# Kernel optimization log

Measured on AMD Instinct MI355X. Metric: run time of the kernel, lower is better.

The kernel has to match this reference:

```python
import jax, jax.numpy as jnp
import numpy as np
import math

D_MODEL = 256
D_STATE = 16
D_CONV = 4
EXPAND = 2
D_INNER = EXPAND * D_MODEL          # 512
DT_RANK = math.ceil(D_MODEL / 16)   # 16
EPS = 1e-5


def rmsnorm(x, w):
    return x * jax.lax.rsqrt(jnp.mean(x * x, axis=-1, keepdims=True) + EPS) * w


def mamba_mixer(x, in_proj, conv_w, conv_b, x_proj, dt_w, dt_b, A_log, Dp, out_proj):
    # x: [B, L, d_model]
    Bsz, L, _ = x.shape
    xz = x @ in_proj.T                       # [B, L, 2*d_inner]
    xh, z = jnp.split(xz, 2, axis=-1)        # each [B, L, d_inner]
    # causal depthwise conv1d over time (d_conv=4)
    xp = jnp.pad(xh, ((0, 0), (D_CONV - 1, 0), (0, 0)))
    xc = sum(xp[:, k:k + L, :] * conv_w[:, k] for k in range(D_CONV)) + conv_b
    xc = jax.nn.silu(xc)                     # [B, L, d_inner]
    x_dbl = xc @ x_proj.T                    # [B, L, dt_rank + 2*d_state]
    dt, Bm, Cm = jnp.split(x_dbl, [DT_RANK, DT_RANK + D_STATE], axis=-1)
    delta = jax.nn.softplus(dt @ dt_w.T + dt_b)   # [B, L, d_inner]
    A = -jnp.exp(A_log)                      # [d_inner, d_state]
    dA = jnp.exp(jnp.einsum('bld,dn->lbdn', delta, A))        # [L,B,d,n]
    dBu = jnp.einsum('bld,bln,bld->lbdn', delta, Bm, xc)       # [L,B,d,n]

    def step(h, inp):
        a, b = inp
        h = a * h + b
        return h, h

    h0 = jnp.zeros((Bsz, D_INNER, D_STATE), xc.dtype)
    _, hs = jax.lax.scan(step, h0, (dA, dBu))                  # [L,B,d,n]
    y = jnp.einsum('lbdn,bln->bld', hs, Cm) + xc * Dp          # [B,L,d_inner]
    y = y * jax.nn.silu(z)
    return y @ out_proj.T                                      # [B,L,d_model]


def block(x, norm_w, in_proj, conv_w, conv_b, x_proj, dt_w, dt_b, A_log, Dp, out_proj):
    # Block with fused_add_norm=False, residual=None: residual = x, h = mixer(norm(x))
    residual = x
    h = mamba_mixer(rmsnorm(x, norm_w), in_proj, conv_w, conv_b, x_proj,
                    dt_w, dt_b, A_log, Dp, out_proj)
    return h + residual


def setup_inputs() -> dict:
    key = jax.random.key(0)
    ks = jax.random.split(key, 16)
    B, L = 4, 2048

    def n(k, shape, s=0.02):
        return jax.random.normal(k, shape, jnp.float32) * s

    inp = {"x": jax.random.normal(ks[0], (B, L, D_MODEL), jnp.float32)}
    i = 1
    for pre in ("fw", "bw"):
        inp[pre + "_norm"] = jnp.ones((D_MODEL,), jnp.float32)
        inp[pre + "_in_proj"] = n(ks[i], (2 * D_INNER, D_MODEL)); i += 1
        inp[pre + "_conv_w"] = n(ks[i], (D_INNER, D_CONV), 0.1); i += 1
        inp[pre + "_conv_b"] = jnp.zeros((D_INNER,), jnp.float32)
        inp[pre + "_x_proj"] = n(ks[i], (DT_RANK + 2 * D_STATE, D_INNER)); i += 1
        inp[pre + "_dt_w"] = n(ks[i], (D_INNER, DT_RANK), 0.1); i += 1
        inp[pre + "_dt_b"] = n(ks[i], (D_INNER,), 0.1); i += 1
        inp[pre + "_A_log"] = jnp.log(jnp.tile(jnp.arange(1, D_STATE + 1, dtype=jnp.float32), (D_INNER, 1)))
        inp[pre + "_D"] = jnp.ones((D_INNER,), jnp.float32)
        inp[pre + "_out_proj"] = n(ks[i], (D_MODEL, D_INNER)); i += 1
    return inp


def reference(x,
              fw_norm, fw_in_proj, fw_conv_w, fw_conv_b, fw_x_proj, fw_dt_w, fw_dt_b, fw_A_log, fw_D, fw_out_proj,
              bw_norm, bw_in_proj, bw_conv_w, bw_conv_b, bw_x_proj, bw_dt_w, bw_dt_b, bw_A_log, bw_D, bw_out_proj):
    fwd = block(x, fw_norm, fw_in_proj, fw_conv_w, fw_conv_b, fw_x_proj,
                fw_dt_w, fw_dt_b, fw_A_log, fw_D, fw_out_proj)
    xb = jnp.flip(x, axis=1)
    bwd = block(xb, bw_norm, bw_in_proj, bw_conv_w, bw_conv_b, bw_x_proj,
                bw_dt_w, bw_dt_b, bw_A_log, bw_D, bw_out_proj)
    bwd = jnp.flip(bwd, axis=1)
    return fwd + bwd
```

## Files before the change

kernel.cpp:

```cpp
#include <hip/hip_runtime.h>
#include <hip/hip_bf16.h>
#include <math.h>


#define NTOK 8192
#define LL   2048
#define DM   256
#define DI   512
#define DS2  16
#define CL   64
#define NCH  32
#define PLANE 65536
#define KSTEP 64

typedef __bf16 bf16x8 __attribute__((ext_vector_type(8)));
typedef float f32x4 __attribute__((ext_vector_type(4)));

__device__ inline unsigned short f2bf(float f) {
    unsigned u = __float_as_uint(f);
    unsigned r = (u + 0x7fffu + ((u >> 16) & 1u)) >> 16;
    return (unsigned short)r;
}
__device__ inline float bf2f(unsigned short s) {
    return __uint_as_float((unsigned)s << 16);
}

#define L2E 1.4426950408889634f
#define LN2 0.6931471805599453f

__device__ inline float softplus_fast(float x) {
    float e = __builtin_amdgcn_exp2f(-fabsf(x) * L2E);
    float l = __builtin_amdgcn_logf(1.f + e);
    return fmaxf(x, 0.f) + l * LN2;
}

__device__ inline int xcd_swz(int bid, int nwg) {
    int q = nwg >> 3, r = nwg & 7;
    int xcd = bid & 7, lo = bid >> 3;
    return (xcd < r ? xcd * (q + 1) : r * (q + 1) + (xcd - r) * q) + lo;
}

#define GLDS(gp, lp) __builtin_amdgcn_global_load_lds( \
    (const __attribute__((address_space(1))) void*)(gp), \
    (__attribute__((address_space(3))) void*)(lp), 16, 0, 0)

__global__ __launch_bounds__(256) void prep_kernel(
    const float* __restrict__ ip0, const float* __restrict__ nw0,
    const float* __restrict__ ip1, const float* __restrict__ nw1,
    const float* __restrict__ xp0, const float* __restrict__ dtw0,
    const float* __restrict__ xp1, const float* __restrict__ dtw1,
    const float* __restrict__ op0, const float* __restrict__ op1,
    unsigned short* __restrict__ w_in, unsigned short* __restrict__ w_p2,
    unsigned short* __restrict__ w_out,
    const float* __restrict__ x, unsigned short* __restrict__ xn) {
    int bid = blockIdx.x, tid = threadIdx.x;
    if (bid < 2048) {
        int dir = bid >> 10, n = bid & 1023;
        const float* ip = dir ? ip1 : ip0;
        const float* nw = dir ? nw1 : nw0;
        w_in[(size_t)bid * 256 + tid] = f2bf(ip[n * 256 + tid] * nw[tid]);
    } else if (bid < 3200) {
        int idx = bid - 2048;
        int dir = idx / 576, row = idx % 576;
        const float* xp = dir ? xp1 : xp0;
        const float* dtw = dir ? dtw1 : dtw0;
        unsigned short* dst = w_p2 + (size_t)idx * 512;
        for (int k = tid; k < 512; k += 256) {
            float v = 0.f;
            if (row < 512) {
                #pragma unroll
                for (int r = 0; r < 16; ++r) v = fmaf(dtw[row * 16 + r], xp[r * 512 + k], v);
            } else if (row < 544) {
                v = xp[(16 + row - 512) * 512 + k];
            }
            dst[k] = f2bf(v);
        }
    } else if (bid < 3456) {
        int n = bid - 3200;
        for (int k = tid; k < 1024; k += 256) {
            float v = (k < 512) ? op0[n * 512 + k] : op1[n * 512 + (k - 512)];
            w_out[(size_t)n * 1024 + k] = f2bf(v);
        }
    } else {
        int t = bid - 3456;
        float v = x[(size_t)t * DM + tid];
        float ss = v * v;
        #pragma unroll
        for (int m = 1; m < 64; m <<= 1) ss += __shfl_xor(ss, m);
        __shared__ float ws[4];
        if ((tid & 63) == 0) ws[tid >> 6] = ss;
        __syncthreads();
        float tot = ws[0] + ws[1] + ws[2] + ws[3];
        float scale = rsqrtf(tot / (float)DM + 1e-5f);
        xn[(size_t)t * DM + tid] = f2bf(v * scale);
    }
}

#define EPI_IN  0
#define EPI_P2  1
#define EPI_OUT 2

template <int EPI>
__global__ __launch_bounds__(256, 3) void mfma_gemm(
    const unsigned short* __restrict__ A0, const unsigned short* __restrict__ A1,
    const unsigned short* __restrict__ Wb, int K,
    unsigned short* __restrict__ d0, unsigned short* __restrict__ d1,
    unsigned short* __restrict__ e0, unsigned short* __restrict__ e1,
    const float* __restrict__ aux0, const float* __restrict__ aux1,
    const float* __restrict__ Xres, float* __restrict__ outF) {
    __shared__ char lds[2][24576];
    int tid = threadIdx.x;
    int lane = tid & 63, wid = tid >> 6;
    int wm = wid >> 1, wn = wid & 1;
    int nwg = gridDim.x * gridDim.y;
    int lid = xcd_swz(blockIdx.y * gridDim.x + blockIdx.x, nwg);
    int n0 = (lid % gridDim.x) * 64;
    int m0 = (lid / gridDim.x) * 128;
    int dir = blockIdx.z;
    const unsigned short* A = dir ? A1 : A0;
    const unsigned short* W = Wb + ((EPI == EPI_P2) ? (size_t)dir * 576 * 512 : 0);

    f32x4 acc[4][2] = {};
    int nt = K / KSTEP;

    auto stage = [&](int t, int buf) {
        int k0 = t * KSTEP;
        char* base = &lds[buf][0];
        #pragma unroll
        for (int i = 0; i < 4; ++i) {
            int s = i * 256 + tid;
            int r = s >> 3, cd = (s & 7) ^ (r & 7);
            GLDS(A + (size_t)(m0 + r) * K + k0 + cd * 8, base + i * 4096 + wid * 1024);
        }
        #pragma unroll
        for (int i = 0; i < 2; ++i) {
            int s = i * 256 + tid;
            int r = s >> 3, cd = (s & 7) ^ (r & 7);
            GLDS(W + (size_t)(n0 + r) * K + k0 + cd * 8, base + 16384 + i * 4096 + wid * 1024);
        }
    };

    stage(0, 0);
    for (int t = 0; t < nt; ++t) {
        int buf = t & 1;
        __syncthreads();
        if (t + 1 < nt) stage(t + 1, buf ^ 1);
        const char* Ab = &lds[buf][0];
        const char* Bb = &lds[buf][16384];
        bf16x8 af[4][2], bfv[2][2];
        #pragma unroll
        for (int mf = 0; mf < 4; ++mf)
            #pragma unroll
            for (int kf = 0; kf < 2; ++kf) {
                int r = wm * 64 + mf * 16 + (lane & 15);
                int c = (lane >> 4) + kf * 4;
                af[mf][kf] = *(const bf16x8*)(Ab + r * 128 + ((c ^ (r & 7)) << 4));
            }
        #pragma unroll
        for (int nf = 0; nf < 2; ++nf)
            #pragma unroll
            for (int kf = 0; kf < 2; ++kf) {
                int r = wn * 32 + nf * 16 + (lane & 15);
                int c = (lane >> 4) + kf * 4;
                bfv[nf][kf] = *(const bf16x8*)(Bb + r * 128 + ((c ^ (r & 7)) << 4));
            }
        #pragma unroll
        for (int kf = 0; kf < 2; ++kf)
            #pragma unroll
            for (int mf = 0; mf < 4; ++mf)
                #pragma unroll
                for (int nf = 0; nf < 2; ++nf)
                    acc[mf][nf] = __builtin_amdgcn_mfma_f32_16x16x32_bf16(
                        af[mf][kf], bfv[nf][kf], acc[mf][nf], 0, 0, 0);
    }

    int cb0 = n0 + wn * 32 + (lane & 15);
    int rb0 = m0 + wm * 64 + ((lane >> 4) << 2);
    #pragma unroll
    for (int mf = 0; mf < 4; ++mf)
        #pragma unroll
        for (int nf = 0; nf < 2; ++nf) {
            int n = cb0 + nf * 16;
            #pragma unroll
            for (int r = 0; r < 4; ++r) {
                int m = rb0 + mf * 16 + r;
                float v = acc[mf][nf][r];
                if (EPI == EPI_IN) {
                    d0[(size_t)m * 2048 + n] = f2bf(v);
                } else if (EPI == EPI_P2) {
                    if (n < 512) {
                        float sv = v + (dir ? aux1 : aux0)[n];
                        (dir ? d1 : d0)[(size_t)m * 512 + n] = f2bf(softplus_fast(sv));
                    } else if (n < 544) {
                        (dir ? e1 : e0)[(size_t)m * 32 + (n - 512)] = f2bf(v);
                    }
                } else {
                    outF[(size_t)m * 256 + n] = v + 2.f * Xres[(size_t)m * 256 + n];
                }
            }
        }
}

__global__ __launch_bounds__(256) void conv_silu_kernel(
    const unsigned short* __restrict__ xz,
    const float* __restrict__ cw0, const float* __restrict__ cw1,
    const float* __restrict__ cb0, const float* __restrict__ cb1,
    unsigned short* __restrict__ o0, unsigned short* __restrict__ o1) {
    int dir = blockIdx.y;
    const float* cw = dir ? cw1 : cw0;
    const float* cb = dir ? cb1 : cb0;
    unsigned short* xc = dir ? o1 : o0;
    int idx8 = blockIdx.x * 256 + threadIdx.x;
    int t = idx8 >> 6;
    int c8 = (idx8 & 63) << 3;
    int l = t & (LL - 1);
    const unsigned short* xh = xz + (size_t)dir * 1024 + c8;

    float wreg[32];
    #pragma unroll
    for (int q = 0; q < 8; ++q)
        *(float4*)&wreg[q * 4] = *(const float4*)&cw[c8 * 4 + q * 4];
    float acc[8];
    *(float4*)&acc[0] = *(const float4*)&cb[c8];
    *(float4*)&acc[4] = *(const float4*)&cb[c8 + 4];

    #pragma unroll
    for (int k = 0; k < 4; ++k) {
        int lo = dir ? (l + 3 - k) : (l - 3 + k);
        if (lo < 0 || lo >= LL) continue;
        uint4 u = *(const uint4*)(xh + (size_t)(t + lo - l) * 2048);
        unsigned wv[4] = {u.x, u.y, u.z, u.w};
        #pragma unroll
        for (int j = 0; j < 4; ++j) {
            float flo = __uint_as_float(wv[j] << 16);
            float fhi = __uint_as_float(wv[j] & 0xffff0000u);
            acc[2 * j]     = fmaf(flo, wreg[(2 * j) * 4 + k], acc[2 * j]);
            acc[2 * j + 1] = fmaf(fhi, wreg[(2 * j + 1) * 4 + k], acc[2 * j + 1]);
        }
    }
    unsigned out[4];
    #pragma unroll
    for (int j = 0; j < 4; ++j) {
        float a0 = acc[2 * j], a1 = acc[2 * j + 1];
        float s0 = a0 / (1.f + __expf(-a0));
        float s1 = a1 / (1.f + __expf(-a1));
        out[j] = (unsigned)f2bf(s0) | ((unsigned)f2bf(s1) << 16);
    }
    *(uint4*)(xc + (size_t)idx8 * 8) = make_uint4(out[0], out[1], out[2], out[3]);
}

__global__ __launch_bounds__(256, 4) void scan_part1(
    const unsigned short* __restrict__ dlt0, const unsigned short* __restrict__ dlt1,
    const unsigned short* __restrict__ xc0, const unsigned short* __restrict__ xc1,
    const unsigned short* __restrict__ bc0, const unsigned short* __restrict__ bc1,
    const float* __restrict__ Al0, const float* __restrict__ Al1,
    const float* __restrict__ Dp0, const float* __restrict__ Dp1,
    float* __restrict__ AC, float* __restrict__ HC,
    unsigned* __restrict__ yls0, unsigned* __restrict__ yls1) {
    int dir = blockIdx.z;
    const unsigned short* delta = dir ? dlt1 : dlt0;
    const unsigned short* xc    = dir ? xc1 : xc0;
    const unsigned short* bc    = dir ? bc1 : bc0;
    const float* Alog           = dir ? Al1 : Al0;
    const float* Dp             = dir ? Dp1 : Dp0;
    unsigned* yls               = dir ? yls1 : yls0;
    int b = blockIdx.y >> 5, ch = blockIdx.y & 31;
    int d0 = blockIdx.x * 128;
    int tid = threadIdx.x;
    int dg = tid >> 1, nq = tid & 1;
    int d = d0 + dg;

    __shared__ unsigned sdxu[CL][128];
    __shared__ unsigned sBC[CL][16];
    {
        int row = tid >> 2, q = tid & 3;
        int lr = ch * CL + row;
        int l = dir ? (LL - 1 - lr) : lr;
        size_t t = (size_t)b * LL + l;
        const uint4* dp = (const uint4*)(delta + t * DI + d0);
        const uint4* xp = (const uint4*)(xc + t * DI + d0);
        #pragma unroll
        for (int hh = 0; hh < 4; ++hh) {
            uint4 du = dp[hh * 4 + q], xu = xp[hh * 4 + q];
            unsigned dw[4] = {du.x, du.y, du.z, du.w};
            unsigned xw[4] = {xu.x, xu.y, xu.z, xu.w};
            #pragma unroll
            for (int j = 0; j < 4; ++j) {
                int col = hh * 32 + q * 8 + 2 * j;
                sdxu[row][col ^ row]       = (dw[j] & 0xffffu) | (xw[j] << 16);
                sdxu[row][(col + 1) ^ row] = (dw[j] >> 16) | (xw[j] & 0xffff0000u);
            }
        }
        uint2 Bu = *(const uint2*)(bc + t * 32 + q * 4);
        uint2 Cu = *(const uint2*)(bc + t * 32 + 16 + q * 4);
        *(uint4*)&sBC[row][q * 4] = make_uint4(
            (Bu.x & 0xffffu) | (Cu.x << 16), (Bu.x >> 16) | (Cu.x & 0xffff0000u),
            (Bu.y & 0xffffu) | (Cu.y << 16), (Bu.y >> 16) | (Cu.y & 0xffff0000u));
    }
    __syncthreads();

    float Av[8], Avl[8];
    {
        float4 Ala = *(const float4*)&Alog[d * DS2 + nq * 8];
        float4 Alb = *(const float4*)&Alog[d * DS2 + nq * 8 + 4];
        Av[0] = -__expf(Ala.x); Av[1] = -__expf(Ala.y);
        Av[2] = -__expf(Ala.z); Av[3] = -__expf(Ala.w);
        Av[4] = -__expf(Alb.x); Av[5] = -__expf(Alb.y);
        Av[6] = -__expf(Alb.z); Av[7] = -__expf(Alb.w);
    }
    #pragma unroll
    for (int j = 0; j < 8; ++j) Avl[j] = Av[j] * L2E;
    bool fast = true;
    #pragma unroll
    for (int j = 0; j < 7; ++j)
        fast = fast && (fabsf(Av[j + 1] - Av[j] + 1.f) < 1e-2f);

    float Dv = Dp[d];
    float h[8] = {0.f, 0.f, 0.f, 0.f, 0.f, 0.f, 0.f, 0.f};
    float sdl = 0.f;
    const float nL2E = -L2E;

    if (fast) {
        #pragma unroll 2
        for (int r = 0; r < CL; ++r) {
            unsigned u = sdxu[r][dg ^ r];
            float dl = __uint_as_float(u << 16);
            float xcv = __uint_as_float(u & 0xffff0000u);
            uint4 q0 = *(const uint4*)&sBC[r][nq * 8];
            uint4 q1 = *(const uint4*)&sBC[r][nq * 8 + 4];
            unsigned bw[8] = {q0.x, q0.y, q0.z, q0.w, q1.x, q1.y, q1.z, q1.w};
            float u0 = dl * xcv;
            sdl += dl;
            float e0 = __builtin_amdgcn_exp2f(dl * Avl[0]);
            float rr = __builtin_amdgcn_exp2f(dl * nL2E);
            float rr2 = rr * rr, rr4 = rr2 * rr2;
            float e[8];
            e[0] = e0;        e[1] = e0 * rr;
            e[2] = e0 * rr2;  e[3] = e[1] * rr2;
            e[4] = e0 * rr4;  e[5] = e[1] * rr4;
            e[6] = e[2] * rr4; e[7] = e[3] * rr4;
            float tsa = 0.f, tsb = 0.f;
            #pragma unroll
            for (int j = 0; j < 8; ++j) {
                float Bf = __uint_as_float(bw[j] << 16);
                float Cf = __uint_as_float(bw[j] & 0xffff0000u);
                h[j] = fmaf(e[j], h[j], u0 * Bf);
                if (j & 1) tsb = fmaf(h[j], Cf, tsb);
                else       tsa = fmaf(h[j], Cf, tsa);
            }
            float ts = tsa + tsb;
            ts += __shfl_xor(ts, 1);
            if (nq == 0) {
                int lr = ch * CL + r;
                float yv = fmaf(xcv, Dv, ts);
                yls[((size_t)b * LL + lr) * DI + d] =
                    (unsigned)f2bf(yv) | ((unsigned)f2bf(sdl) << 16);
            }
        }
    } else {
        #pragma unroll 2
        for (int r = 0; r < CL; ++r) {
            unsigned u = sdxu[r][dg ^ r];
            float dl = __uint_as_float(u << 16);
            float xcv = __uint_as_float(u & 0xffff0000u);
            uint4 q0 = *(const uint4*)&sBC[r][nq * 8];
            uint4 q1 = *(const uint4*)&sBC[r][nq * 8 + 4];
            unsigned bw[8] = {q0.x, q0.y, q0.z, q0.w, q1.x, q1.y, q1.z, q1.w};
            float u0 = dl * xcv;
            sdl += dl;
            float ts = 0.f;
            #pragma unroll
            for (int j = 0; j < 8; ++j) {
                float Bf = __uint_as_float(bw[j] << 16);
                float Cf = __uint_as_float(bw[j] & 0xffff0000u);
                float e = __builtin_amdgcn_exp2f(dl * Avl[j]);
                h[j] = fmaf(e, h[j], u0 * Bf);
                ts = fmaf(h[j], Cf, ts);
            }
            ts += __shfl_xor(ts, 1);
            if (nq == 0) {
                int lr = ch * CL + r;
                float yv = fmaf(xcv, Dv, ts);
                yls[((size_t)b * LL + lr) * DI + d] =
                    (unsigned)f2bf(yv) | ((unsigned)f2bf(sdl) << 16);
            }
        }
    }

    size_t base = (size_t)ch * PLANE + (size_t)(((dir * 4 + b) * DI + d) * DS2 + nq * 8);
    float ac[8];
    #pragma unroll
    for (int j = 0; j < 8; ++j) ac[j] = __builtin_amdgcn_exp2f(Avl[j] * sdl);
    *(float4*)&AC[base]     = make_float4(ac[0], ac[1], ac[2], ac[3]);
    *(float4*)&AC[base + 4] = make_float4(ac[4], ac[5], ac[6], ac[7]);
    *(float4*)&HC[base]     = make_float4(h[0], h[1], h[2], h[3]);
    *(float4*)&HC[base + 4] = make_float4(h[4], h[5], h[6], h[7]);
}

__global__ __launch_bounds__(256) void scan_part2(
    const float* __restrict__ AC, const float* __restrict__ HC,
    float* __restrict__ HIN) {
    int idx = blockIdx.x * 256 + threadIdx.x;
    float hin = 0.f;
    #pragma unroll
    for (int ch = 0; ch < NCH; ++ch) {
        size_t o = (size_t)ch * PLANE + idx;
        HIN[o] = hin;
        hin = fmaf(AC[o], hin, HC[o]);
    }
}

__global__ __launch_bounds__(256, 8) void scan_lite(
    const unsigned* __restrict__ yls0, const unsigned* __restrict__ yls1,
    const unsigned short* __restrict__ bc0, const unsigned short* __restrict__ bc1,
    const unsigned short* __restrict__ xz,
    const float* __restrict__ Al0, const float* __restrict__ Al1,
    const float* __restrict__ HIN, unsigned short* __restrict__ ycat) {
    int dir = blockIdx.z;
    const unsigned* yls         = dir ? yls1 : yls0;
    const unsigned short* bc    = dir ? bc1 : bc0;
    const float* Alog           = dir ? Al1 : Al0;
    int b = blockIdx.y >> 5, ch = blockIdx.y & 31;
    int d0 = blockIdx.x * 64;
    int tid = threadIdx.x;
    int dg = tid & 63, lg = tid >> 6;
    int d = d0 + dg;

    __shared__ unsigned sC[CL][8];
    {
        int row = tid >> 2, q = tid & 3;
        if (q < 2) {
            int lr = ch * CL + row;
            int l = dir ? (LL - 1 - lr) : lr;
            size_t t = (size_t)b * LL + l;
            uint4 cu = *(const uint4*)(bc + t * 32 + 16 + q * 8);
            *(uint4*)&sC[row][q * 4] = cu;
        }
    }
    __syncthreads();

    float Av[16];
    bool fastA = true;
    #pragma unroll
    for (int qq = 0; qq < 4; ++qq) {
        float4 Al = *(const float4*)&Alog[d * DS2 + qq * 4];
        Av[qq * 4 + 0] = -__expf(Al.x);
        Av[qq * 4 + 1] = -__expf(Al.y);
        Av[qq * 4 + 2] = -__expf(Al.z);
        Av[qq * 4 + 3] = -__expf(Al.w);
    }
    #pragma unroll
    for (int n = 0; n < 16; ++n)
        fastA = fastA && (fabsf(Av[n] + (float)(n + 1)) < 1e-3f * (float)(n + 1));

    float hin[16];
    size_t hbase = (size_t)ch * PLANE + (size_t)(((dir * 4 + b) * DI + d) * DS2);
    #pragma unroll
    for (int qq = 0; qq < 4; ++qq)
        *(float4*)&hin[qq * 4] = *(const float4*)&HIN[hbase + qq * 4];

    #pragma unroll 2
    for (int i = 0; i < 16; ++i) {
        int row = lg * 16 + i;
        int lr = ch * CL + row;
        int ll = dir ? (LL - 1 - lr) : lr;
        size_t tt = (size_t)b * LL + ll;
        unsigned u = yls[((size_t)b * LL + lr) * DI + d];
        float yv = __uint_as_float(u << 16);
        float s  = __uint_as_float(u & 0xffff0000u);
        if (fastA) {
            float E = __builtin_amdgcn_exp2f(-s * L2E);
            if (__any(E > 3e-6f)) {
                float acc = 0.f;
                #pragma unroll
                for (int p = 7; p >= 0; --p) {
                    unsigned cp = sC[row][p];
                    float C0 = __uint_as_float(cp << 16);
                    float C1 = __uint_as_float(cp & 0xffff0000u);
                    acc = fmaf(acc, E, C1 * hin[2 * p + 1]);
                    acc = fmaf(acc, E, C0 * hin[2 * p]);
                }
                yv = fmaf(acc, E, yv);
            }
        } else {
            float acc = 0.f;
            #pragma unroll
            for (int p = 0; p < 8; ++p) {
                unsigned cp = sC[row][p];
                float C0 = __uint_as_float(cp << 16);
                float C1 = __uint_as_float(cp & 0xffff0000u);
                float e0 = __builtin_amdgcn_exp2f(s * Av[2 * p] * L2E);
                float e1 = __builtin_amdgcn_exp2f(s * Av[2 * p + 1] * L2E);
                acc = fmaf(e0 * hin[2 * p], C0, acc);
                acc = fmaf(e1 * hin[2 * p + 1], C1, acc);
            }
            yv += acc;
        }
        float zz = bf2f(xz[tt * 2048 + (size_t)dir * 1024 + 512 + d]);
        yv *= zz / (1.f + __expf(-zz));
        ycat[tt * 1024 + (size_t)dir * 512 + d] = f2bf(yv);
    }
}

extern "C" void kernel_launch(void* const* d_in, const int* in_sizes, int n_in,
                              void* d_out, int out_size, void* d_ws, size_t ws_size,
                              hipStream_t stream) {
    const float* x = (const float*)d_in[0];
    const float* p[2][10];
    for (int dir = 0; dir < 2; ++dir)
        for (int i = 0; i < 10; ++i)
            p[dir][i] = (const float*)d_in[1 + dir * 10 + i];

    char* w = (char*)d_ws;
    auto alloc = [&](size_t bytes) { char* q = w; w += (bytes + 255) & ~(size_t)255; return q; };
    unsigned short* xn    = (unsigned short*)alloc((size_t)NTOK * DM * 2);
    unsigned short* w_in  = (unsigned short*)alloc((size_t)2048 * 256 * 2);
    unsigned short* w_p2  = (unsigned short*)alloc((size_t)1152 * 512 * 2);
    unsigned short* w_out = (unsigned short*)alloc((size_t)256 * 1024 * 2);
    unsigned short* xzcat = (unsigned short*)alloc((size_t)NTOK * 2048 * 2);
    unsigned short *xcb[2], *dlt[2], *bc[2];
    unsigned* yls[2];
    for (int dir = 0; dir < 2; ++dir) {
        xcb[dir] = (unsigned short*)alloc((size_t)NTOK * DI * 2);
        dlt[dir] = (unsigned short*)alloc((size_t)NTOK * DI * 2);
        bc[dir]  = (unsigned short*)alloc((size_t)NTOK * 32 * 2);
        yls[dir] = (unsigned*)alloc((size_t)NTOK * DI * 4);
    }
    unsigned short* ycat = (unsigned short*)alloc((size_t)NTOK * 1024 * 2);
    float* AC  = (float*)alloc((size_t)NCH * PLANE * 4);
    float* HC  = (float*)alloc((size_t)NCH * PLANE * 4);
    float* HIN = (float*)alloc((size_t)NCH * PLANE * 4);
    float* out = (float*)d_out;

    prep_kernel<<<3456 + NTOK, 256, 0, stream>>>(
        p[0][1], p[0][0], p[1][1], p[1][0],
        p[0][4], p[0][5], p[1][4], p[1][5],
        p[0][9], p[1][9], w_in, w_p2, w_out, x, xn);

    mfma_gemm<EPI_IN><<<dim3(32, 64, 1), 256, 0, stream>>>(
        xn, xn, w_in, 256, xzcat, nullptr, nullptr, nullptr,
        nullptr, nullptr, nullptr, nullptr);

    conv_silu_kernel<<<dim3(2048, 2), 256, 0, stream>>>(
        xzcat, p[0][2], p[1][2], p[0][3], p[1][3], xcb[0], xcb[1]);

    mfma_gemm<EPI_P2><<<dim3(9, 64, 2), 256, 0, stream>>>(
        xcb[0], xcb[1], w_p2, 512, dlt[0], dlt[1], bc[0], bc[1],
        p[0][6], p[1][6], nullptr, nullptr);

    scan_part1<<<dim3(DI / 128, 4 * NCH, 2), 256, 0, stream>>>(
        dlt[0], dlt[1], xcb[0], xcb[1], bc[0], bc[1], p[0][7], p[1][7],
        p[0][8], p[1][8], AC, HC, yls[0], yls[1]);
    scan_part2<<<PLANE / 256, 256, 0, stream>>>(AC, HC, HIN);
    scan_lite<<<dim3(DI / 64, 4 * NCH, 2), 256, 0, stream>>>(
        yls[0], yls[1], bc[0], bc[1], xzcat,
        p[0][7], p[1][7], HIN, ycat);

    mfma_gemm<EPI_OUT><<<dim3(4, 64, 1), 256, 0, stream>>>(
        ycat, ycat, w_out, 1024, nullptr, nullptr, nullptr, nullptr,
        nullptr, nullptr, x, out);
}
```

Before: 171.8 us.

## Switch GEMM to 64x64 tiles with K=256 single-buffered stages

The MFMA GEMM drops from 128x64 output tiles with double-buffered K=64 stages to 64x64 tiles that load a whole K=256 slab into 64KB of LDS per stage, with no double buffering. Grids double in M so there are more workgroups, and launch bounds fall to 2 waves per SIMD. The goal is fewer barriers and more parallelism across CUs. In exchange, each tile reuses its inputs less, loads no longer overlap compute, and occupancy drops because of the larger LDS footprint.

```diff
diff --git a/kernel.cpp b/kernel.cpp
--- a/kernel.cpp
+++ b/kernel.cpp
@@ -11,7 +11,6 @@
 #define CL   64
 #define NCH  32
 #define PLANE 65536
-#define KSTEP 64
 
 typedef __bf16 bf16x8 __attribute__((ext_vector_type(8)));
 typedef float f32x4 __attribute__((ext_vector_type(4)));
@@ -101,83 +100,68 @@
 #define EPI_OUT 2
 
 template <int EPI>
-__global__ __launch_bounds__(256, 3) void mfma_gemm(
+__global__ __launch_bounds__(256, 2) void mfma_gemm(
     const unsigned short* __restrict__ A0, const unsigned short* __restrict__ A1,
     const unsigned short* __restrict__ Wb, int K,
     unsigned short* __restrict__ d0, unsigned short* __restrict__ d1,
     unsigned short* __restrict__ e0, unsigned short* __restrict__ e1,
     const float* __restrict__ aux0, const float* __restrict__ aux1,
     const float* __restrict__ Xres, float* __restrict__ outF) {
-    __shared__ char lds[2][24576];
+    __shared__ char lds[2][32768];
     int tid = threadIdx.x;
     int lane = tid & 63, wid = tid >> 6;
     int wm = wid >> 1, wn = wid & 1;
     int nwg = gridDim.x * gridDim.y;
     int lid = xcd_swz(blockIdx.y * gridDim.x + blockIdx.x, nwg);
     int n0 = (lid % gridDim.x) * 64;
-    int m0 = (lid / gridDim.x) * 128;
+    int m0 = (lid / gridDim.x) * 64;
     int dir = blockIdx.z;
     const unsigned short* A = dir ? A1 : A0;
     const unsigned short* W = Wb + ((EPI == EPI_P2) ? (size_t)dir * 576 * 512 : 0);
 
-    f32x4 acc[4][2] = {};
-    int nt = K / KSTEP;
-
-    auto stage = [&](int t, int buf) {
-        int k0 = t * KSTEP;
-        char* base = &lds[buf][0];
+    f32x4 acc[2][2] = {};
+    int nt = K >> 8;
+
+    for (int p = 0; p < nt; ++p) {
+        if (p) __syncthreads();
+        int k0 = p << 8;
         #pragma unroll
-        for (int i = 0; i < 4; ++i) {
+        for (int i = 0; i < 8; ++i) {
             int s = i * 256 + tid;
-            int r = s >> 3, cd = (s & 7) ^ (r & 7);
-            GLDS(A + (size_t)(m0 + r) * K + k0 + cd * 8, base + i * 4096 + wid * 1024);
-        }
+            int r = s >> 5, cs = (s & 31) ^ (r & 7);
+            GLDS(A + (size_t)(m0 + r) * K + k0 + cs * 8, &lds[0][0] + i * 4096 + wid * 1024);
+            GLDS(W + (size_t)(n0 + r) * K + k0 + cs * 8, &lds[1][0] + i * 4096 + wid * 1024);
+        }
+        __syncthreads();
+        const char* Ab = &lds[0][0];
+        const char* Bb = &lds[1][0];
         #pragma unroll
-        for (int i = 0; i < 2; ++i) {
-            int s = i * 256 + tid;
-            int r = s >> 3, cd = (s & 7) ^ (r & 7);
-            GLDS(W + (size_t)(n0 + r) * K + k0 + cd * 8, base + 16384 + i * 4096 + wid * 1024);
-        }
-    };
-
-    stage(0, 0);
-    for (int t = 0; t < nt; ++t) {
-        int buf = t & 1;
-        __syncthreads();
-        if (t + 1 < nt) stage(t + 1, buf ^ 1);
-        const char* Ab = &lds[buf][0];
-        const char* Bb = &lds[buf][16384];
-        bf16x8 af[4][2], bfv[2][2];
-        #pragma unroll
-        for (int mf = 0; mf < 4; ++mf)
-            #pragma unroll
-            for (int kf = 0; kf < 2; ++kf) {
-                int r = wm * 64 + mf * 16 + (lane & 15);
-                int c = (lane >> 4) + kf * 4;
-                af[mf][kf] = *(const bf16x8*)(Ab + r * 128 + ((c ^ (r & 7)) << 4));
-            }
-        #pragma unroll
-        for (int nf = 0; nf < 2; ++nf)
-            #pragma unroll
-            for (int kf = 0; kf < 2; ++kf) {
+        for (int kf = 0; kf < 8; ++kf) {
+            bf16x8 af[2], bfv[2];
+            int c = (lane >> 4) + kf * 4;
+            #pragma unroll
+            for (int mf = 0; mf < 2; ++mf) {
+                int r = wm * 32 + mf * 16 + (lane & 15);
+                af[mf] = *(const bf16x8*)(Ab + r * 512 + ((c ^ (r & 7)) << 4));
+            }
+            #pragma unroll
+            for (int nf = 0; nf < 2; ++nf) {
                 int r = wn * 32 + nf * 16 + (lane & 15);
-                int c = (lane >> 4) + kf * 4;
-                bfv[nf][kf] = *(const bf16x8*)(Bb + r * 128 + ((c ^ (r & 7)) << 4));
-            }
-        #pragma unroll
-        for (int kf = 0; kf < 2; ++kf)
-            #pragma unroll
-            for (int mf = 0; mf < 4; ++mf)
+                bfv[nf] = *(const bf16x8*)(Bb + r * 512 + ((c ^ (r & 7)) << 4));
+            }
+            #pragma unroll
+            for (int mf = 0; mf < 2; ++mf)
                 #pragma unroll
                 for (int nf = 0; nf < 2; ++nf)
                     acc[mf][nf] = __builtin_amdgcn_mfma_f32_16x16x32_bf16(
-                        af[mf][kf], bfv[nf][kf], acc[mf][nf], 0, 0, 0);
+                        af[mf], bfv[nf], acc[mf][nf], 0, 0, 0);
+        }
     }
 
     int cb0 = n0 + wn * 32 + (lane & 15);
-    int rb0 = m0 + wm * 64 + ((lane >> 4) << 2);
-    #pragma unroll
-    for (int mf = 0; mf < 4; ++mf)
+    int rb0 = m0 + wm * 32 + ((lane >> 4) << 2);
+    #pragma unroll
+    for (int mf = 0; mf < 2; ++mf)
         #pragma unroll
         for (int nf = 0; nf < 2; ++nf) {
             int n = cb0 + nf * 16;
@@ -335,9 +319,9 @@
             float rr = __builtin_amdgcn_exp2f(dl * nL2E);
             float rr2 = rr * rr, rr4 = rr2 * rr2;
             float e[8];
-            e[0] = e0;        e[1] = e0 * rr;
-            e[2] = e0 * rr2;  e[3] = e[1] * rr2;
-            e[4] = e0 * rr4;  e[5] = e[1] * rr4;
+            e[0] = e0;         e[1] = e0 * rr;
+            e[2] = e0 * rr2;   e[3] = e[1] * rr2;
+            e[4] = e0 * rr4;   e[5] = e[1] * rr4;
             e[6] = e[2] * rr4; e[7] = e[3] * rr4;
             float tsa = 0.f, tsb = 0.f;
             #pragma unroll
@@ -537,14 +521,14 @@
         p[0][4], p[0][5], p[1][4], p[1][5],
         p[0][9], p[1][9], w_in, w_p2, w_out, x, xn);
 
-    mfma_gemm<EPI_IN><<<dim3(32, 64, 1), 256, 0, stream>>>(
+    mfma_gemm<EPI_IN><<<dim3(32, 128, 1), 256, 0, stream>>>(
         xn, xn, w_in, 256, xzcat, nullptr, nullptr, nullptr,
         nullptr, nullptr, nullptr, nullptr);
 
     conv_silu_kernel<<<dim3(2048, 2), 256, 0, stream>>>(
         xzcat, p[0][2], p[1][2], p[0][3], p[1][3], xcb[0], xcb[1]);
 
-    mfma_gemm<EPI_P2><<<dim3(9, 64, 2), 256, 0, stream>>>(
+    mfma_gemm<EPI_P2><<<dim3(9, 128, 2), 256, 0, stream>>>(
         xcb[0], xcb[1], w_p2, 512, dlt[0], dlt[1], bc[0], bc[1],
         p[0][6], p[1][6], nullptr, nullptr);
 
@@ -556,7 +540,7 @@
         yls[0], yls[1], bc[0], bc[1], xzcat,
         p[0][7], p[1][7], HIN, ycat);
 
-    mfma_gemm<EPI_OUT><<<dim3(4, 64, 1), 256, 0, stream>>>(
+    mfma_gemm<EPI_OUT><<<dim3(4, 128, 1), 256, 0, stream>>>(
         ycat, ycat, w_out, 1024, nullptr, nullptr, nullptr, nullptr,
         nullptr, nullptr, x, out);
 }
```

New measurement: 179.6 us. 4.5% more time.
